# Kernel optimization log

Measured on AMD Instinct MI355X. Metric: run time of the kernel, lower is better.

Reference implementation:

```python
import jax, jax.numpy as jnp
import numpy as np

N, C_IN, C_OUT, H, W = 8, 128, 64, 128, 128
KH, KW, DILATE = 9, 9, 2


def _shifted(xp, dh, dw, dilate, Hh, Ww):
    # xp: zero-padded [N,C,H+2ph,W+2pw]; returns window-offset (dh,dw) view [N,C,H,W]
    return xp[:, :, dh * dilate:dh * dilate + Hh, dw * dilate:dw * dilate + Ww]


def local_similar(q, k, kH, kW, dilate):
    # q,k: [N,C,H,W] -> logits [N,H,W,kH*kW]
    n, c, h, w = q.shape
    ph, pw = dilate * (kH // 2), dilate * (kW // 2)
    kp = jnp.pad(k, ((0, 0), (0, 0), (ph, ph), (pw, pw)))
    outs = []
    for dh in range(kH):
        for dw in range(kW):
            ks = _shifted(kp, dh, dw, dilate, h, w)
            outs.append(jnp.einsum('nchw,nchw->nhw', q, ks))
    return jnp.stack(outs, axis=-1)


def local_weighting(v, wgt, kH, kW, dilate):
    # v: [N,C,H,W], wgt: [N,H,W,kH*kW] -> [N,C,H,W]
    n, c, h, w = v.shape
    ph, pw = dilate * (kH // 2), dilate * (kW // 2)
    vp = jnp.pad(v, ((0, 0), (0, 0), (ph, ph), (pw, pw)))
    out = jnp.zeros_like(v)
    idx = 0
    for dh in range(kH):
        for dw in range(kW):
            vs = _shifted(vp, dh, dw, dilate, h, w)
            out = out + vs * wgt[..., idx][:, None, :, :]
            idx += 1
    return out


def setup_inputs() -> dict:
    key = jax.random.key(0)
    kx, k1, k2, k3 = jax.random.split(key, 4)
    s = 1.0 / np.sqrt(C_IN)
    return {
        'x': jax.random.normal(kx, (N, C_IN, H, W), dtype=jnp.float32),
        'W1': jax.random.normal(k1, (C_OUT, C_IN), dtype=jnp.float32) * s,
        'W2': jax.random.normal(k2, (C_OUT, C_IN), dtype=jnp.float32) * s,
        'W3': jax.random.normal(k3, (C_OUT, C_IN), dtype=jnp.float32) * s,
    }


def reference(x, W1, W2, W3):
    # 1x1 convs (no bias)
    x1 = jnp.einsum('oc,nchw->nohw', W1, x)
    x2 = jnp.einsum('oc,nchw->nohw', W2, x)
    x3 = jnp.einsum('oc,nchw->nohw', W3, x)
    logits = local_similar(x1, x2, KH, KW, DILATE)      # [N,H,W,kH*kW]
    weight = jax.nn.softmax(logits, axis=-1)
    out = local_weighting(x3, weight, KH, KW, DILATE)   # [N,C_out,H,W]
    return out
```

## Files before the change

kernel.cpp:

```cpp
#include <hip/hip_runtime.h>
#include <cstdint>
#include <cstddef>

#define NB   8
#define CIN  128
#define COUT 64
#define NPIX 131072
#define PLANE NPIX
#define LOG2E 1.44269504088896340736f

typedef _Float16 f16;
typedef _Float16 half4_t __attribute__((ext_vector_type(4)));
typedef _Float16 half8_t __attribute__((ext_vector_type(8)));
typedef short    bs8    __attribute__((ext_vector_type(8)));
typedef float    float4_t __attribute__((ext_vector_type(4)));
typedef unsigned int uint2_t __attribute__((ext_vector_type(2)));

__device__ __forceinline__ unsigned short f2bf(float f){
  unsigned u = __float_as_uint(f);
  return (unsigned short)((u + 0x7fffu + ((u >> 16) & 1u)) >> 16);
}

__global__ __launch_bounds__(256) void wsetup_k(
    const float* __restrict__ W1, const float* __restrict__ W2,
    const float* __restrict__ W3, f16* __restrict__ Wf)
{
  int idx = blockIdx.x * 256 + threadIdx.x;
  int mat = idx >> 13;
  int rem = idx & 8191;
  const float* src = (mat == 0 ? W1 : (mat == 1 ? W2 : W3));
  float v = src[rem];
  if (mat == 0) v *= LOG2E;
  Wf[idx] = (f16)v;
}

__global__ __launch_bounds__(256, 4) void conv_mfma_k(
    const float* __restrict__ x, const f16* __restrict__ Wf,
    f16* __restrict__ Qi, f16* __restrict__ Ki, unsigned short* __restrict__ V2)
{
  __shared__ __align__(16) f16 xs[2][64 * 136];

  int tid = threadIdx.x, lane = tid & 63, wv = tid >> 6;
  int l15 = lane & 15, q4 = lane >> 4;
  int b = blockIdx.x;
  int vb = (b & 7) * 128 + (b >> 3);
  int pxt = vb * 128;
  int n = pxt >> 14, hwt = pxt & 16383;

  int pxi = lane & 15, cg = lane >> 4;

  float4_t pre[2][4];
  auto load_regs = [&](int co) {
    #pragma unroll
    for (int s = 0; s < 2; ++s) {
      int c4 = s * 16 + wv * 4 + cg;
      const float* xp = x + ((size_t)(n * CIN + c4 * 4) << 14) + hwt + co + pxi * 4;
      pre[s][0] = *(const float4_t*)(xp);
      pre[s][1] = *(const float4_t*)(xp + 16384);
      pre[s][2] = *(const float4_t*)(xp + 32768);
      pre[s][3] = *(const float4_t*)(xp + 49152);
    }
  };
  auto write_lds = [&](int buf) {
    #pragma unroll
    for (int s = 0; s < 2; ++s) {
      int c4 = s * 16 + wv * 4 + cg;
      #pragma unroll
      for (int i = 0; i < 4; ++i) {
        half4_t h = { (f16)pre[s][0][i], (f16)pre[s][1][i],
                      (f16)pre[s][2][i], (f16)pre[s][3][i] };
        *(half4_t*)&xs[buf][(pxi * 4 + i) * 136 + c4 * 4] = h;
      }
    }
  };

  half8_t wq[4], wk[4], wvf[4];
  #pragma unroll
  for (int k0 = 0; k0 < 4; ++k0) {
    wq[k0]  = *(const half8_t*)&Wf[((wv     )*16 + l15)*128 + k0*32 + q4*8];
    wk[k0]  = *(const half8_t*)&Wf[((wv +  4)*16 + l15)*128 + k0*32 + q4*8];
    wvf[k0] = *(const half8_t*)&Wf[((wv +  8)*16 + l15)*128 + k0*32 + q4*8];
  }

  auto compute = [&](int buf, int co) {
    #pragma unroll
    for (int mt = 0; mt < 4; ++mt) {
      float4_t cq = {0.f,0.f,0.f,0.f}, ck = {0.f,0.f,0.f,0.f}, cv = {0.f,0.f,0.f,0.f};
      #pragma unroll
      for (int k0 = 0; k0 < 4; ++k0) {
        half8_t xa = *(half8_t*)&xs[buf][(mt*16 + l15)*136 + k0*32 + q4*8];
        cq = __builtin_amdgcn_mfma_f32_16x16x32_f16(wq[k0],  xa, cq, 0, 0, 0);
        ck = __builtin_amdgcn_mfma_f32_16x16x32_f16(wk[k0],  xa, ck, 0, 0, 0);
        cv = __builtin_amdgcn_mfma_f32_16x16x32_f16(xa, wvf[k0], cv, 0, 0, 0);
      }
      int pxq = pxt + co + mt*16 + l15;
      int g   = wv*2 + (q4 >> 1);
      half4_t hq = {(f16)cq[0], (f16)cq[1], (f16)cq[2], (f16)cq[3]};
      half4_t hk = {(f16)ck[0], (f16)ck[1], (f16)ck[2], (f16)ck[3]};
      *(half4_t*)&Qi[((size_t)g * PLANE + pxq) * 8 + (q4 & 1)*4] = hq;
      *(half4_t*)&Ki[((size_t)g * PLANE + pxq) * 8 + (q4 & 1)*4] = hk;
      uint2_t pv;
      pv.x = (unsigned)f2bf(cv[0]) | ((unsigned)f2bf(cv[1]) << 16);
      pv.y = (unsigned)f2bf(cv[2]) | ((unsigned)f2bf(cv[3]) << 16);
      *(uint2_t*)&V2[(size_t)(wv*16 + l15) * PLANE + pxt + co + mt*16 + q4*4] = pv;
    }
  };

  load_regs(0);
  write_lds(0);
  load_regs(64);
  __syncthreads();
  compute(0, 0);
  write_lds(1);
  __syncthreads();
  compute(1, 64);
}

__global__ __launch_bounds__(512, 4) void attn_fused_k(
    const f16* __restrict__ Qi, const f16* __restrict__ Ki,
    const unsigned short* __restrict__ V2, float* __restrict__ out)
{
  __shared__ __align__(16) unsigned short plds[8][2][16 * 40];

  int tid = threadIdx.x, lane = tid & 63, wv = tid >> 6;
  int l15 = lane & 15, q4 = lane >> 4;
  int b = blockIdx.x;
  int n = b & 7;
  int p = b >> 3;
  int h0 = (p >> 1)*4 + (p & 1);
  int h2 = h0 + 2;
  int seg = wv * 16;
  int nb = n << 14;

  unsigned short* P0 = &plds[wv][0][0];
  unsigned short* P1 = &plds[wv][1][0];

  half8_t aq0[2], aq1[2];
  {
    int px0 = nb + (h0 << 7) + seg + l15;
    aq0[0] = *(const half8_t*)&Qi[((size_t)(q4    ) * PLANE + px0) * 8];
    aq0[1] = *(const half8_t*)&Qi[((size_t)(q4 + 4) * PLANE + px0) * 8];
    int px1 = px0 + 256;
    aq1[0] = *(const half8_t*)&Qi[((size_t)(q4    ) * PLANE + px1) * 8];
    aq1[1] = *(const half8_t*)&Qi[((size_t)(q4 + 4) * PLANE + px1) * 8];
  }

  unsigned vbits = 0;
  #pragma unroll
  for (int jt = 0; jt < 2; ++jt)
    #pragma unroll
    for (int rr = 0; rr < 4; ++rr) {
      int jw = seg - 8 + jt*16 + q4*4 + rr;
      int iw = seg + l15;
      int d  = jw - iw;
      bool val = (((d & 1) == 0) & (d >= -8) & (d <= 8) & ((unsigned)jw < 128u));
      vbits |= ((unsigned)val) << (jt*4 + rr);
    }

  float s0 = 0.f, s1 = 0.f;
  float4_t o0[4], o1[4];
  #pragma unroll
  for (int ct = 0; ct < 4; ++ct) {
    o0[ct] = (float4_t){0.f,0.f,0.f,0.f};
    o1[ct] = (float4_t){0.f,0.f,0.f,0.f};
  }

  auto row_body = [&](const half8_t* aq, float& s_part,
                      float4_t* o, unsigned short* P,
                      const half8_t (&bk)[2][2], const bs8 (&bv)[4]) {
    float4_t st0 = (float4_t){0.f,0.f,0.f,0.f};
    float4_t st1 = (float4_t){0.f,0.f,0.f,0.f};
    st0 = __builtin_amdgcn_mfma_f32_16x16x32_f16(bk[0][0], aq[0], st0, 0, 0, 0);
    st0 = __builtin_amdgcn_mfma_f32_16x16x32_f16(bk[0][1], aq[1], st0, 0, 0, 0);
    st1 = __builtin_amdgcn_mfma_f32_16x16x32_f16(bk[1][0], aq[0], st1, 0, 0, 0);
    st1 = __builtin_amdgcn_mfma_f32_16x16x32_f16(bk[1][1], aq[1], st1, 0, 0, 0);
    #pragma unroll
    for (int rr = 0; rr < 4; ++rr) {
      st0[rr] = exp2f(((vbits >> rr)       & 1u) ? st0[rr] : -1e30f);
      st1[rr] = exp2f(((vbits >> (4 + rr)) & 1u) ? st1[rr] : -1e30f);
    }
    s_part += (st0[0] + st0[1]) + (st0[2] + st0[3])
            + (st1[0] + st1[1]) + (st1[2] + st1[3]);
    uint2_t pk0, pk1;
    pk0.x = (__float_as_uint(st0[1]) & 0xffff0000u) | (__float_as_uint(st0[0]) >> 16);
    pk0.y = (__float_as_uint(st0[3]) & 0xffff0000u) | (__float_as_uint(st0[2]) >> 16);
    pk1.x = (__float_as_uint(st1[1]) & 0xffff0000u) | (__float_as_uint(st1[0]) >> 16);
    pk1.y = (__float_as_uint(st1[3]) & 0xffff0000u) | (__float_as_uint(st1[2]) >> 16);
    *(uint2_t*)&P[l15*40      + q4*4] = pk0;
    *(uint2_t*)&P[l15*40 + 16 + q4*4] = pk1;
    bs8 ap = *(bs8*)&P[l15*40 + q4*8];
    #pragma unroll
    for (int ct = 0; ct < 4; ++ct)
      o[ct] = __builtin_amdgcn_mfma_f32_16x16x32_bf16(ap, bv[ct], o[ct], 0, 0, 0);
  };

  for (int hs = h0 - 8; hs <= h0 + 10; hs += 2) {
    if (hs < 0 || hs > 127) continue;
    int jbase = nb + (hs << 7) + seg - 8;

    half8_t bk[2][2];
    #pragma unroll
    for (int jt = 0; jt < 2; ++jt) {
      int pxj = jbase + jt*16 + l15;
      bk[jt][0] = *(const half8_t*)&Ki[((size_t)(q4    ) * PLANE + pxj) * 8];
      bk[jt][1] = *(const half8_t*)&Ki[((size_t)(q4 + 4) * PLANE + pxj) * 8];
    }
    bs8 bv[4];
    #pragma unroll
    for (int ct = 0; ct < 4; ++ct)
      bv[ct] = *(const bs8*)&V2[(size_t)(ct*16 + l15) * PLANE + jbase + q4*8];

    if (hs <= h0 + 8) row_body(aq0, s0, o0, P0, bk, bv);
    if (hs >= h2 - 8) row_body(aq1, s1, o1, P1, bk, bv);
  }

  int iw = seg + l15;
  int wlo = iw - 8; if (wlo < 0) wlo = 0;
  int whi = iw + 8; if (whi > 127) whi = 127;
  int vw = ((whi - wlo) >> 1) + 1;
  #pragma unroll
  for (int row = 0; row < 2; ++row) {
    int hr = row ? h2 : h0;
    int hlo = hr - 8; if (hlo < 0) hlo = 0;
    int hhi = hr + 8; if (hhi > 127) hhi = 127;
    int vh = ((hhi - hlo) >> 1) + 1;
    float cnt = (float)(81 - vh * vw);
    float srow = row ? s1 : s0;
    srow += __shfl_xor(srow, 16, 64);
    srow += __shfl_xor(srow, 32, 64);
    float sc = 1.f / (srow + cnt);
    float4_t scv;
    #pragma unroll
    for (int rr = 0; rr < 4; ++rr) scv[rr] = __shfl(sc, q4*4 + rr, 64);
    const float4_t* o = row ? o1 : o0;
    #pragma unroll
    for (int ct = 0; ct < 4; ++ct) {
      size_t ob = ((size_t)(n*COUT + ct*16 + l15) << 14) + (hr << 7) + seg + q4*4;
      float4_t stv;
      #pragma unroll
      for (int rr = 0; rr < 4; ++rr) stv[rr] = o[ct][rr] * scv[rr];
      *(float4_t*)&out[ob] = stv;
    }
  }
}

extern "C" void kernel_launch(void* const* d_in, const int* in_sizes, int n_in,
                              void* d_out, int out_size, void* d_ws, size_t ws_size,
                              hipStream_t stream)
{
  const float* x  = (const float*)d_in[0];
  const float* W1 = (const float*)d_in[1];
  const float* W2 = (const float*)d_in[2];
  const float* W3 = (const float*)d_in[3];

  f16* Wf = (f16*)d_ws;
  f16* Qi = (f16*)((char*)d_ws + 65536);
  f16* Ki = Qi + (size_t)8 * PLANE * 8;
  unsigned short* V2 = (unsigned short*)(Ki + (size_t)8 * PLANE * 8);

  float* outp = (float*)d_out;

  wsetup_k    <<<96,        256, 0, stream>>>(W1, W2, W3, Wf);
  conv_mfma_k <<<NPIX/128,  256, 0, stream>>>(x, Wf, Qi, Ki, V2);
  attn_fused_k<<<NB*128/2,  512, 0, stream>>>(Qi, Ki, V2, outp);
}
```

Before: 154.4 us.

## Switch attention kernel to 32x32 MFMA with permlane32 swap instead of LDS

Rewrites the fused local-attention kernel to process both query rows at once with 32x32x16 MFMA tiles instead of 16x16x32 tiles. The probability tile is now moved from the QK output layout into the PV input layout with permlane32_swap in registers, which removes the per-wave LDS staging buffer and its write/read round trip. The loop bounds are computed up front rather than skipped per iteration. The cost is 16-wide accumulators (more VGPR pressure) and some wasted work on masked rows at the image boundary.

```diff
diff --git a/kernel.cpp b/kernel.cpp
--- a/kernel.cpp
+++ b/kernel.cpp
@@ -14,6 +14,7 @@
 typedef _Float16 half8_t __attribute__((ext_vector_type(8)));
 typedef short    bs8    __attribute__((ext_vector_type(8)));
 typedef float    float4_t __attribute__((ext_vector_type(4)));
+typedef float    f32x16  __attribute__((ext_vector_type(16)));
 typedef unsigned int uint2_t __attribute__((ext_vector_type(2)));
 
 __device__ __forceinline__ unsigned short f2bf(float f){
@@ -120,125 +121,125 @@
     const f16* __restrict__ Qi, const f16* __restrict__ Ki,
     const unsigned short* __restrict__ V2, float* __restrict__ out)
 {
-  __shared__ __align__(16) unsigned short plds[8][2][16 * 40];
-
   int tid = threadIdx.x, lane = tid & 63, wv = tid >> 6;
-  int l15 = lane & 15, q4 = lane >> 4;
+  int col = lane & 31, hsel = lane >> 5;
   int b = blockIdx.x;
-  int n = b & 7;
+  int img = b & 7;
   int p = b >> 3;
   int h0 = (p >> 1)*4 + (p & 1);
   int h2 = h0 + 2;
   int seg = wv * 16;
-  int nb = n << 14;
-
-  unsigned short* P0 = &plds[wv][0][0];
-  unsigned short* P1 = &plds[wv][1][0];
-
-  half8_t aq0[2], aq1[2];
+  int nb = img << 14;
+
+  half8_t aq[4];
   {
-    int px0 = nb + (h0 << 7) + seg + l15;
-    aq0[0] = *(const half8_t*)&Qi[((size_t)(q4    ) * PLANE + px0) * 8];
-    aq0[1] = *(const half8_t*)&Qi[((size_t)(q4 + 4) * PLANE + px0) * 8];
-    int px1 = px0 + 256;
-    aq1[0] = *(const half8_t*)&Qi[((size_t)(q4    ) * PLANE + px1) * 8];
-    aq1[1] = *(const half8_t*)&Qi[((size_t)(q4 + 4) * PLANE + px1) * 8];
+    int pxn = nb + (((col < 16) ? h0 : h2) << 7) + seg + (col & 15);
+    #pragma unroll
+    for (int k = 0; k < 4; ++k)
+      aq[k] = *(const half8_t*)&Qi[((size_t)(k*2 + hsel) * PLANE + pxn) * 8];
   }
 
   unsigned vbits = 0;
-  #pragma unroll
-  for (int jt = 0; jt < 2; ++jt)
-    #pragma unroll
-    for (int rr = 0; rr < 4; ++rr) {
-      int jw = seg - 8 + jt*16 + q4*4 + rr;
-      int iw = seg + l15;
+  {
+    int iw = seg + (col & 15);
+    #pragma unroll
+    for (int r = 0; r < 16; ++r) {
+      int jj = (r & 3) + 8*(r >> 2) + 4*hsel;
+      int jw = seg - 8 + jj;
       int d  = jw - iw;
       bool val = (((d & 1) == 0) & (d >= -8) & (d <= 8) & ((unsigned)jw < 128u));
-      vbits |= ((unsigned)val) << (jt*4 + rr);
-    }
-
-  float s0 = 0.f, s1 = 0.f;
-  float4_t o0[4], o1[4];
+      vbits |= ((unsigned)val) << r;
+    }
+  }
+
+  float s = 0.f;
+  f32x16 o0, o1;
   #pragma unroll
-  for (int ct = 0; ct < 4; ++ct) {
-    o0[ct] = (float4_t){0.f,0.f,0.f,0.f};
-    o1[ct] = (float4_t){0.f,0.f,0.f,0.f};
-  }
-
-  auto row_body = [&](const half8_t* aq, float& s_part,
-                      float4_t* o, unsigned short* P,
-                      const half8_t (&bk)[2][2], const bs8 (&bv)[4]) {
-    float4_t st0 = (float4_t){0.f,0.f,0.f,0.f};
-    float4_t st1 = (float4_t){0.f,0.f,0.f,0.f};
-    st0 = __builtin_amdgcn_mfma_f32_16x16x32_f16(bk[0][0], aq[0], st0, 0, 0, 0);
-    st0 = __builtin_amdgcn_mfma_f32_16x16x32_f16(bk[0][1], aq[1], st0, 0, 0, 0);
-    st1 = __builtin_amdgcn_mfma_f32_16x16x32_f16(bk[1][0], aq[0], st1, 0, 0, 0);
-    st1 = __builtin_amdgcn_mfma_f32_16x16x32_f16(bk[1][1], aq[1], st1, 0, 0, 0);
-    #pragma unroll
-    for (int rr = 0; rr < 4; ++rr) {
-      st0[rr] = exp2f(((vbits >> rr)       & 1u) ? st0[rr] : -1e30f);
-      st1[rr] = exp2f(((vbits >> (4 + rr)) & 1u) ? st1[rr] : -1e30f);
-    }
-    s_part += (st0[0] + st0[1]) + (st0[2] + st0[3])
-            + (st1[0] + st1[1]) + (st1[2] + st1[3]);
-    uint2_t pk0, pk1;
-    pk0.x = (__float_as_uint(st0[1]) & 0xffff0000u) | (__float_as_uint(st0[0]) >> 16);
-    pk0.y = (__float_as_uint(st0[3]) & 0xffff0000u) | (__float_as_uint(st0[2]) >> 16);
-    pk1.x = (__float_as_uint(st1[1]) & 0xffff0000u) | (__float_as_uint(st1[0]) >> 16);
-    pk1.y = (__float_as_uint(st1[3]) & 0xffff0000u) | (__float_as_uint(st1[2]) >> 16);
-    *(uint2_t*)&P[l15*40      + q4*4] = pk0;
-    *(uint2_t*)&P[l15*40 + 16 + q4*4] = pk1;
-    bs8 ap = *(bs8*)&P[l15*40 + q4*8];
-    #pragma unroll
-    for (int ct = 0; ct < 4; ++ct)
-      o[ct] = __builtin_amdgcn_mfma_f32_16x16x32_bf16(ap, bv[ct], o[ct], 0, 0, 0);
-  };
-
-  for (int hs = h0 - 8; hs <= h0 + 10; hs += 2) {
-    if (hs < 0 || hs > 127) continue;
-    int jbase = nb + (hs << 7) + seg - 8;
-
-    half8_t bk[2][2];
-    #pragma unroll
-    for (int jt = 0; jt < 2; ++jt) {
-      int pxj = jbase + jt*16 + l15;
-      bk[jt][0] = *(const half8_t*)&Ki[((size_t)(q4    ) * PLANE + pxj) * 8];
-      bk[jt][1] = *(const half8_t*)&Ki[((size_t)(q4 + 4) * PLANE + pxj) * 8];
-    }
-    bs8 bv[4];
-    #pragma unroll
-    for (int ct = 0; ct < 4; ++ct)
-      bv[ct] = *(const bs8*)&V2[(size_t)(ct*16 + l15) * PLANE + jbase + q4*8];
-
-    if (hs <= h0 + 8) row_body(aq0, s0, o0, P0, bk, bv);
-    if (hs >= h2 - 8) row_body(aq1, s1, o1, P1, bk, bv);
-  }
-
-  int iw = seg + l15;
+  for (int r = 0; r < 16; ++r) { o0[r] = 0.f; o1[r] = 0.f; }
+
+  int lo = (h0 >= 8) ? (h0 - 8) : (h0 & 1);
+  int hi = (h0 + 10 <= 127) ? (h0 + 10) : (126 + (h0 & 1));
+
+  for (int hs = lo; hs <= hi; hs += 2) {
+    int jb = nb + (hs << 7) + seg - 8;
+
+    half8_t bk[4];
+    #pragma unroll
+    for (int k = 0; k < 4; ++k)
+      bk[k] = *(const half8_t*)&Ki[((size_t)(k*2 + hsel) * PLANE + jb + col) * 8];
+    bs8 bvv[2][2];
+    #pragma unroll
+    for (int ks = 0; ks < 2; ++ks)
+      #pragma unroll
+      for (int ct = 0; ct < 2; ++ct)
+        bvv[ks][ct] = *(const bs8*)&V2[(size_t)(ct*32 + col) * PLANE + jb + ks*16 + hsel*8];
+
+    f32x16 st;
+    #pragma unroll
+    for (int r = 0; r < 16; ++r) st[r] = 0.f;
+    #pragma unroll
+    for (int k = 0; k < 4; ++k)
+      st = __builtin_amdgcn_mfma_f32_32x32x16_f16(bk[k], aq[k], st, 0, 0, 0);
+
+    bool rok = (col < 16) ? (hs <= h0 + 8) : (hs >= h2 - 8);
+    unsigned em = rok ? vbits : 0u;
+    #pragma unroll
+    for (int r = 0; r < 16; ++r) {
+      st[r] = exp2f(((em >> r) & 1u) ? st[r] : -1e30f);
+      s += st[r];
+    }
+
+    unsigned pq[8];
+    #pragma unroll
+    for (int q = 0; q < 8; ++q)
+      pq[q] = (__float_as_uint(st[2*q+1]) & 0xffff0000u) | (__float_as_uint(st[2*q]) >> 16);
+
+    uint2_t w0 = __builtin_amdgcn_permlane32_swap(pq[0], pq[2], false, false);
+    uint2_t w1 = __builtin_amdgcn_permlane32_swap(pq[1], pq[3], false, false);
+    uint2_t w2 = __builtin_amdgcn_permlane32_swap(pq[4], pq[6], false, false);
+    uint2_t w3 = __builtin_amdgcn_permlane32_swap(pq[5], pq[7], false, false);
+    unsigned pa0u[4] = { w0.x, w1.x, w0.y, w1.y };
+    unsigned pa1u[4] = { w2.x, w3.x, w2.y, w3.y };
+    bs8 pa0, pa1;
+    #pragma unroll
+    for (int q = 0; q < 4; ++q) {
+      pa0[2*q]   = (short)(pa0u[q] & 0xffffu);
+      pa0[2*q+1] = (short)(pa0u[q] >> 16);
+      pa1[2*q]   = (short)(pa1u[q] & 0xffffu);
+      pa1[2*q+1] = (short)(pa1u[q] >> 16);
+    }
+
+    o0 = __builtin_amdgcn_mfma_f32_32x32x16_bf16(pa0, bvv[0][0], o0, 0, 0, 0);
+    o0 = __builtin_amdgcn_mfma_f32_32x32x16_bf16(pa1, bvv[1][0], o0, 0, 0, 0);
+    o1 = __builtin_amdgcn_mfma_f32_32x32x16_bf16(pa0, bvv[0][1], o1, 0, 0, 0);
+    o1 = __builtin_amdgcn_mfma_f32_32x32x16_bf16(pa1, bvv[1][1], o1, 0, 0, 0);
+  }
+
+  float srow = s + __shfl_xor(s, 32, 64);
+  int iw = seg + (col & 15);
   int wlo = iw - 8; if (wlo < 0) wlo = 0;
   int whi = iw + 8; if (whi > 127) whi = 127;
   int vw = ((whi - wlo) >> 1) + 1;
+  int hr = (col < 16) ? h0 : h2;
+  int hlo = hr - 8; if (hlo < 0) hlo = 0;
+  int hhi = hr + 8; if (hhi > 127) hhi = 127;
+  int vh = ((hhi - hlo) >> 1) + 1;
+  float cnt = (float)(81 - vh * vw);
+  float sc = 1.f / (srow + cnt);
+
   #pragma unroll
-  for (int row = 0; row < 2; ++row) {
-    int hr = row ? h2 : h0;
-    int hlo = hr - 8; if (hlo < 0) hlo = 0;
-    int hhi = hr + 8; if (hhi > 127) hhi = 127;
-    int vh = ((hhi - hlo) >> 1) + 1;
-    float cnt = (float)(81 - vh * vw);
-    float srow = row ? s1 : s0;
-    srow += __shfl_xor(srow, 16, 64);
-    srow += __shfl_xor(srow, 32, 64);
-    float sc = 1.f / (srow + cnt);
-    float4_t scv;
-    #pragma unroll
-    for (int rr = 0; rr < 4; ++rr) scv[rr] = __shfl(sc, q4*4 + rr, 64);
-    const float4_t* o = row ? o1 : o0;
-    #pragma unroll
-    for (int ct = 0; ct < 4; ++ct) {
-      size_t ob = ((size_t)(n*COUT + ct*16 + l15) << 14) + (hr << 7) + seg + q4*4;
+  for (int ct = 0; ct < 2; ++ct) {
+    const f32x16& o = ct ? o1 : o0;
+    #pragma unroll
+    for (int gp = 0; gp < 4; ++gp) {
+      int m_base = 8*gp + 4*hsel;
+      int hrow  = (m_base >> 4) ? h2 : h0;
+      int i_b   = seg + (m_base & 15);
       float4_t stv;
       #pragma unroll
-      for (int rr = 0; rr < 4; ++rr) stv[rr] = o[ct][rr] * scv[rr];
+      for (int q = 0; q < 4; ++q)
+        stv[q] = o[4*gp + q] * __shfl(sc, m_base + q, 64);
+      size_t ob = ((size_t)(img*COUT + ct*32 + col) << 14) + (hrow << 7) + i_b;
       *(float4_t*)&out[ob] = stv;
     }
   }
```

Result: no change. 155.4 us (+0.6%).
